# Performance work log

Measured on AMD Instinct MI355X. Metric: run time of the kernel, lower is better.

## Reference

```python
import jax, jax.numpy as jnp
import numpy as np

B, T, C, H = 8, 2048, 1024, 64

def setup_inputs() -> dict:
    key = jax.random.key(0)
    k1, k2, k3, k4 = jax.random.split(key, 4)
    x = jax.random.normal(k1, (B, T, C), dtype=jnp.float32)
    # torch nn.Linear default init ~ U(-1/sqrt(in), 1/sqrt(in)); scale kept small for stability
    s = 1.0 / np.sqrt(C)
    Wq = jax.random.uniform(k2, (C, H), dtype=jnp.float32, minval=-s, maxval=s)
    Wk = jax.random.uniform(k3, (C, H), dtype=jnp.float32, minval=-s, maxval=s)
    Wv = jax.random.uniform(k4, (C, H), dtype=jnp.float32, minval=-s, maxval=s)
    return {"x": x, "Wq": Wq, "Wk": Wk, "Wv": Wv}

def reference(x, Wq, Wk, Wv):
    # x: [B,T,C]; Wq/Wk/Wv: [C,H] (equivalent to torch Linear weight transposed)
    Q = jnp.einsum('btc,ch->bth', x, Wq)
    K = jnp.einsum('btc,ch->bth', x, Wk)
    V = jnp.einsum('btc,ch->bth', x, Wv)
    H_ = Q.shape[-1]
    scale = 1.0 / jnp.sqrt(jnp.asarray(H_, dtype=Q.dtype))
    w = jnp.einsum('bqh,bkh->bqk', Q, K) * scale  # [B,T,T]
    T_ = x.shape[1]
    causal = jnp.tril(jnp.ones((T_, T_), dtype=bool))
    w = jnp.where(causal, w, -jnp.inf)
    w = jax.nn.softmax(w, axis=-1)
    out = jnp.einsum('bqk,bkh->bqh', w, V)  # [B,T,H]
    return out
```

## Files before the change

kernel.cpp:

```cpp
#include <hip/hip_runtime.h>
#include <math.h>

#define Bb 8
#define Tt 2048
#define Cc 1024
#define Hh 64
#define BT (Bb * Tt)
#define SLOG2E 0.18033688011112042f

typedef __attribute__((ext_vector_type(8))) short short8;
typedef __attribute__((ext_vector_type(4))) float floatx4;

__device__ inline unsigned short f2bf(float f) {
  unsigned int u = __builtin_bit_cast(unsigned int, f);
  u += 0x7fff + ((u >> 16) & 1);
  return (unsigned short)(u >> 16);
}
__device__ inline float bf2f(unsigned short u) {
  unsigned int x = ((unsigned int)u) << 16;
  return __builtin_bit_cast(float, x);
}

__global__ __launch_bounds__(256) void wconv2(
    const float* __restrict__ Wq, const float* __restrict__ Wk,
    const float* __restrict__ Wv, unsigned short* __restrict__ WTf) {
  int bid = blockIdx.x;
  int w = bid >> 5;
  int kc = bid & 31;
  const float* __restrict__ W = (w == 0) ? Wq : (w == 1 ? Wk : Wv);
  int t = threadIdx.x;
  int hg = t >> 6, quad = (t >> 4) & 3, lrow = t & 15;
  int g = w * 4 + hg;
  int h = hg * 16 + lrow;
  unsigned short tmp[8];
#pragma unroll
  for (int j = 0; j < 8; ++j)
    tmp[j] = f2bf(W[(size_t)(kc * 32 + quad * 8 + j) * Hh + h]);
  unsigned short* dst = &WTf[((size_t)(g * 32 + kc) * 64 + quad * 16 + lrow) * 8];
  *(ushort4*)dst = make_ushort4(tmp[0], tmp[1], tmp[2], tmp[3]);
  *(ushort4*)(dst + 4) = make_ushort4(tmp[4], tmp[5], tmp[6], tmp[7]);
}

__global__ __launch_bounds__(256) void qkv5(
    const float* __restrict__ x, const unsigned short* __restrict__ WTf,
    unsigned short* __restrict__ Qb, unsigned short* __restrict__ Kb,
    unsigned short* __restrict__ VTt) {
  __shared__ __align__(16) unsigned short Af[2048];

  int mt = blockIdx.x;
  int t = threadIdx.x;
  int wv = t >> 6, lane = t & 63;
  int lrow = lane & 15, quad = lane >> 4;

  floatx4 acc[2][3];
#pragma unroll
  for (int g2 = 0; g2 < 2; ++g2)
#pragma unroll
    for (int j = 0; j < 3; ++j)
#pragma unroll
      for (int r = 0; r < 4; ++r) acc[g2][j][r] = 0.f;

  int srow = t >> 3, scg = t & 7;
  int skc2 = scg >> 2, squad = scg & 3;
  int sslot = ((srow >> 4) * 2 + skc2) * 64 + squad * 16 +
              (((srow & 15) + squad + 4 * skc2) & 15);
  const float* xp = x + (size_t)(mt * 32 + srow) * Cc + scg * 8;

  int aslot[2][2];
#pragma unroll
  for (int g2 = 0; g2 < 2; ++g2)
#pragma unroll
    for (int kc2 = 0; kc2 < 2; ++kc2)
      aslot[g2][kc2] = ((g2 * 2 + kc2) * 64 + quad * 16 +
                        ((lrow + quad + 4 * kc2) & 15)) * 8;

  const unsigned short* wbase[3];
#pragma unroll
  for (int j = 0; j < 3; ++j)
    wbase[j] = WTf + (size_t)(wv * 3 + j) * 32 * 512 + lane * 8;

  float4 nv0 = *(const float4*)xp;
  float4 nv1 = *(const float4*)(xp + 4);

  for (int kk = 0; kk < 16; ++kk) {
    __syncthreads();
    short8 a;
    a[0] = (short)f2bf(nv0.x); a[1] = (short)f2bf(nv0.y);
    a[2] = (short)f2bf(nv0.z); a[3] = (short)f2bf(nv0.w);
    a[4] = (short)f2bf(nv1.x); a[5] = (short)f2bf(nv1.y);
    a[6] = (short)f2bf(nv1.z); a[7] = (short)f2bf(nv1.w);
    *(short8*)&Af[sslot * 8] = a;
    if (kk < 15) {
      nv0 = *(const float4*)(xp + (kk + 1) * 64);
      nv1 = *(const float4*)(xp + (kk + 1) * 64 + 4);
    }
    __syncthreads();

    short8 bf[3][2];
    int kg = kk * 2;
#pragma unroll
    for (int j = 0; j < 3; ++j)
#pragma unroll
      for (int kc2 = 0; kc2 < 2; ++kc2)
        bf[j][kc2] = *(const short8*)(wbase[j] + (size_t)(kg + kc2) * 512);
    short8 af[2][2];
#pragma unroll
    for (int g2 = 0; g2 < 2; ++g2)
#pragma unroll
      for (int kc2 = 0; kc2 < 2; ++kc2)
        af[g2][kc2] = *(const short8*)&Af[aslot[g2][kc2]];
#pragma unroll
    for (int g2 = 0; g2 < 2; ++g2)
#pragma unroll
      for (int j = 0; j < 3; ++j) {
        acc[g2][j] = __builtin_amdgcn_mfma_f32_16x16x32_bf16(af[g2][0], bf[j][0], acc[g2][j], 0, 0, 0);
        acc[g2][j] = __builtin_amdgcn_mfma_f32_16x16x32_bf16(af[g2][1], bf[j][1], acc[g2][j], 0, 0, 0);
      }
  }

#pragma unroll
  for (int g2 = 0; g2 < 2; ++g2) {
    int tok0 = mt * 32 + g2 * 16 + quad * 4;
#pragma unroll
    for (int j = 0; j < 3; ++j) {
      int nbase = (wv * 3 + j) * 16;
      if (nbase >= 128) {
        int h = nbase - 128 + lrow;
        *(ushort4*)&VTt[(size_t)(tok0 >> 6) * 4096 + h * 64 + (tok0 & 63)] =
            make_ushort4(f2bf(acc[g2][j][0]), f2bf(acc[g2][j][1]),
                         f2bf(acc[g2][j][2]), f2bf(acc[g2][j][3]));
      } else {
        unsigned short* dst = (nbase >= 64) ? Kb : Qb;
        int col = (nbase & 63) + lrow;
#pragma unroll
        for (int r = 0; r < 4; ++r)
          dst[(size_t)(tok0 + r) * Hh + col] = f2bf(acc[g2][j][r]);
      }
    }
  }
}

__global__ __launch_bounds__(512) void attn3(
    const unsigned short* __restrict__ Qb, const unsigned short* __restrict__ Kb,
    const unsigned short* __restrict__ VTt, float* __restrict__ out) {
  __shared__ __align__(16) unsigned char smem[33 * 1024];
  unsigned short* Pall = (unsigned short*)smem;
  unsigned short* Ocomb = (unsigned short*)smem;
  float* Lcomb = (float*)(smem + 32768);

  int bid = blockIdx.x;
  int b = bid >> 5;
  int j = bid & 31;
  int t = threadIdx.x;
  int wv = t >> 6, lane = t & 63;
  int lrow = lane & 15, quad = lane >> 4;

  unsigned short* Pw = Pall + wv * 2048;

  short8 ones;
#pragma unroll
  for (int i = 0; i < 8; ++i) ones[i] = (short)0x3F80;

  for (int half = 0; half < 2; ++half) {
    int qt = half ? (63 - j) : j;
    int q0 = qt * 32;
    int nkt = (qt >> 1) + 1;

    short8 aq[2][2];
#pragma unroll
    for (int qs = 0; qs < 2; ++qs)
#pragma unroll
      for (int kc = 0; kc < 2; ++kc)
        aq[qs][kc] = *(const short8*)
            &Qb[(size_t)(b * Tt + q0 + qs * 16 + lrow) * Hh + kc * 32 + quad * 8];

    floatx4 acc_o[2][4];
    floatx4 acc_l[2];
#pragma unroll
    for (int qs = 0; qs < 2; ++qs) {
#pragma unroll
      for (int r = 0; r < 4; ++r) acc_l[qs][r] = 0.f;
#pragma unroll
      for (int hs = 0; hs < 4; ++hs)
#pragma unroll
        for (int r = 0; r < 4; ++r) acc_o[qs][hs][r] = 0.f;
    }

    for (int kt = wv; kt < nkt; kt += 8) {
      int kbase = b * Tt + kt * 64;
      short8 kf[4][2], vf[4][2];
#pragma unroll
      for (int sn = 0; sn < 4; ++sn)
#pragma unroll
        for (int kc = 0; kc < 2; ++kc)
          kf[sn][kc] = *(const short8*)
              &Kb[(size_t)(kbase + sn * 16 + lrow) * Hh + kc * 32 + quad * 8];
      int ktile = b * 32 + kt;
#pragma unroll
      for (int hs = 0; hs < 4; ++hs)
#pragma unroll
        for (int kc = 0; kc < 2; ++kc)
          vf[hs][kc] = *(const short8*)
              &VTt[(size_t)ktile * 4096 + (hs * 16 + lrow) * 64 + kc * 32 + quad * 8];

      floatx4 s[2][4];
#pragma unroll
      for (int qs = 0; qs < 2; ++qs)
#pragma unroll
        for (int sn = 0; sn < 4; ++sn) {
          floatx4 z;
#pragma unroll
          for (int r = 0; r < 4; ++r) z[r] = 0.f;
          z = __builtin_amdgcn_mfma_f32_16x16x32_bf16(aq[qs][0], kf[sn][0], z, 0, 0, 0);
          z = __builtin_amdgcn_mfma_f32_16x16x32_bf16(aq[qs][1], kf[sn][1], z, 0, 0, 0);
          s[qs][sn] = z;
        }

      bool diag = (kt == nkt - 1);
#pragma unroll
      for (int qs = 0; qs < 2; ++qs)
#pragma unroll
        for (int sn = 0; sn < 4; ++sn) {
          int k5 = (sn & 1) * 16 + lrow;
          int slot = qs * 2 + (sn >> 1);
          int rlbase = (k5 >> 3) * 16;
#pragma unroll
          for (int r = 0; r < 4; ++r) {
            float v = s[qs][sn][r] * SLOG2E;
            if (diag) {
              int gk = kt * 64 + sn * 16 + lrow;
              int gq = q0 + qs * 16 + quad * 4 + r;
              if (gk > gq) v = -INFINITY;
            }
            float p = exp2f(v);
            Pw[slot * 512 + (rlbase + quad * 4 + r) * 8 + (k5 & 7)] = f2bf(p);
          }
        }

      short8 ap[2][2];
#pragma unroll
      for (int qs = 0; qs < 2; ++qs)
#pragma unroll
        for (int kc = 0; kc < 2; ++kc)
          ap[qs][kc] = *(const short8*)&Pw[(qs * 2 + kc) * 512 + lane * 8];

#pragma unroll
      for (int qs = 0; qs < 2; ++qs) {
        acc_l[qs] = __builtin_amdgcn_mfma_f32_16x16x32_bf16(ap[qs][0], ones, acc_l[qs], 0, 0, 0);
        acc_l[qs] = __builtin_amdgcn_mfma_f32_16x16x32_bf16(ap[qs][1], ones, acc_l[qs], 0, 0, 0);
#pragma unroll
        for (int hs = 0; hs < 4; ++hs) {
          acc_o[qs][hs] = __builtin_amdgcn_mfma_f32_16x16x32_bf16(ap[qs][0], vf[hs][0], acc_o[qs][hs], 0, 0, 0);
          acc_o[qs][hs] = __builtin_amdgcn_mfma_f32_16x16x32_bf16(ap[qs][1], vf[hs][1], acc_o[qs][hs], 0, 0, 0);
        }
      }
    }

#pragma unroll
    for (int qs = 0; qs < 2; ++qs)
#pragma unroll
      for (int hs = 0; hs < 4; ++hs) {
        int s8 = qs * 4 + hs;
        *(ushort4*)&Ocomb[((wv * 8 + s8) * 64 + lane) * 4] =
            make_ushort4(f2bf(acc_o[qs][hs][0]), f2bf(acc_o[qs][hs][1]),
                         f2bf(acc_o[qs][hs][2]), f2bf(acc_o[qs][hs][3]));
      }
    if (lrow == 0) {
#pragma unroll
      for (int qs = 0; qs < 2; ++qs)
#pragma unroll
        for (int r = 0; r < 4; ++r)
          Lcomb[wv * 32 + qs * 16 + quad * 4 + r] = acc_l[qs][r];
    }
    __syncthreads();

    {
      int qsub = wv >> 2, hs = wv & 3;
      float o[4] = {0.f, 0.f, 0.f, 0.f};
#pragma unroll
      for (int w = 0; w < 8; ++w) {
        ushort4 pk = *(const ushort4*)&Ocomb[((w * 8 + wv) * 64 + lane) * 4];
        o[0] += bf2f(pk.x); o[1] += bf2f(pk.y);
        o[2] += bf2f(pk.z); o[3] += bf2f(pk.w);
      }
#pragma unroll
      for (int r = 0; r < 4; ++r) {
        float lv = 0.f;
#pragma unroll
        for (int w = 0; w < 8; ++w)
          lv += Lcomb[w * 32 + qsub * 16 + quad * 4 + r];
        int row = q0 + qsub * 16 + quad * 4 + r;
        out[(size_t)(b * Tt + row) * Hh + hs * 16 + lrow] = o[r] / lv;
      }
    }
    __syncthreads();
  }
}

extern "C" void kernel_launch(void* const* d_in, const int* in_sizes, int n_in,
                              void* d_out, int out_size, void* d_ws, size_t ws_size,
                              hipStream_t stream) {
  const float* x = (const float*)d_in[0];
  const float* Wq = (const float*)d_in[1];
  const float* Wk = (const float*)d_in[2];
  const float* Wv = (const float*)d_in[3];
  float* out = (float*)d_out;

  unsigned short* WTf = (unsigned short*)d_ws;
  unsigned short* Qb = WTf + 192 * 1024;
  unsigned short* Kb = Qb + (size_t)BT * Hh;
  unsigned short* VTt = Kb + (size_t)BT * Hh;

  wconv2<<<dim3(96), dim3(256), 0, stream>>>(Wq, Wk, Wv, WTf);
  qkv5<<<dim3(512), dim3(256), 0, stream>>>(x, WTf, Qb, Kb, VTt);
  attn3<<<dim3(256), dim3(512), 0, stream>>>(Qb, Kb, VTt, out);
}
```

Before: 132.8 us.

## Prefetch two x tiles, use packed bf16 converts, transpose-read P, fold softmax scale

```diff
diff --git a/kernel.cpp b/kernel.cpp
--- a/kernel.cpp
+++ b/kernel.cpp
@@ -9,7 +9,9 @@
 #define SLOG2E 0.18033688011112042f
 
 typedef __attribute__((ext_vector_type(8))) short short8;
+typedef __attribute__((ext_vector_type(4))) short s16x4;
 typedef __attribute__((ext_vector_type(4))) float floatx4;
+typedef __attribute__((ext_vector_type(4))) unsigned int uint4v;
 
 __device__ inline unsigned short f2bf(float f) {
   unsigned int u = __builtin_bit_cast(unsigned int, f);
@@ -79,20 +81,28 @@
   for (int j = 0; j < 3; ++j)
     wbase[j] = WTf + (size_t)(wv * 3 + j) * 32 * 512 + lane * 8;
 
-  float4 nv0 = *(const float4*)xp;
-  float4 nv1 = *(const float4*)(xp + 4);
-
-  for (int kk = 0; kk < 16; ++kk) {
+  float4 va0 = *(const float4*)xp;
+  float4 va1 = *(const float4*)(xp + 4);
+  float4 vb0 = *(const float4*)(xp + 64);
+  float4 vb1 = *(const float4*)(xp + 68);
+
+  auto cvt8 = [](const float4& u, const float4& v) -> short8 {
+    unsigned int p0, p1, p2, p3;
+    asm("v_cvt_pk_bf16_f32 %0, %1, %2" : "=v"(p0) : "v"(u.x), "v"(u.y));
+    asm("v_cvt_pk_bf16_f32 %0, %1, %2" : "=v"(p1) : "v"(u.z), "v"(u.w));
+    asm("v_cvt_pk_bf16_f32 %0, %1, %2" : "=v"(p2) : "v"(v.x), "v"(v.y));
+    asm("v_cvt_pk_bf16_f32 %0, %1, %2" : "=v"(p3) : "v"(v.z), "v"(v.w));
+    uint4v w; w[0] = p0; w[1] = p1; w[2] = p2; w[3] = p3;
+    return __builtin_bit_cast(short8, w);
+  };
+
+  auto step = [&](float4& n0, float4& n1, int kk) {
     __syncthreads();
-    short8 a;
-    a[0] = (short)f2bf(nv0.x); a[1] = (short)f2bf(nv0.y);
-    a[2] = (short)f2bf(nv0.z); a[3] = (short)f2bf(nv0.w);
-    a[4] = (short)f2bf(nv1.x); a[5] = (short)f2bf(nv1.y);
-    a[6] = (short)f2bf(nv1.z); a[7] = (short)f2bf(nv1.w);
+    short8 a = cvt8(n0, n1);
     *(short8*)&Af[sslot * 8] = a;
-    if (kk < 15) {
-      nv0 = *(const float4*)(xp + (kk + 1) * 64);
-      nv1 = *(const float4*)(xp + (kk + 1) * 64 + 4);
+    if (kk + 2 < 16) {
+      n0 = *(const float4*)(xp + (kk + 2) * 64);
+      n1 = *(const float4*)(xp + (kk + 2) * 64 + 4);
     }
     __syncthreads();
 
@@ -116,6 +126,12 @@
         acc[g2][j] = __builtin_amdgcn_mfma_f32_16x16x32_bf16(af[g2][0], bf[j][0], acc[g2][j], 0, 0, 0);
         acc[g2][j] = __builtin_amdgcn_mfma_f32_16x16x32_bf16(af[g2][1], bf[j][1], acc[g2][j], 0, 0, 0);
       }
+  };
+
+#pragma unroll
+  for (int kk2 = 0; kk2 < 8; ++kk2) {
+    step(va0, va1, kk2 * 2);
+    step(vb0, vb1, kk2 * 2 + 1);
   }
 
 #pragma unroll
@@ -131,10 +147,11 @@
                          f2bf(acc[g2][j][2]), f2bf(acc[g2][j][3]));
       } else {
         unsigned short* dst = (nbase >= 64) ? Kb : Qb;
+        float sc = (nbase >= 64) ? 1.0f : SLOG2E;
         int col = (nbase & 63) + lrow;
 #pragma unroll
         for (int r = 0; r < 4; ++r)
-          dst[(size_t)(tok0 + r) * Hh + col] = f2bf(acc[g2][j][r]);
+          dst[(size_t)(tok0 + r) * Hh + col] = f2bf(acc[g2][j][r] * sc);
       }
     }
   }
@@ -156,6 +173,16 @@
   int lrow = lane & 15, quad = lane >> 4;
 
   unsigned short* Pw = Pall + wv * 2048;
+  unsigned int pbase = (unsigned int)(size_t)Pw;
+
+  unsigned int paddr[2][2];
+#pragma unroll
+  for (int qs = 0; qs < 2; ++qs)
+#pragma unroll
+    for (int kc = 0; kc < 2; ++kc)
+      paddr[qs][kc] = pbase + (unsigned int)(qs * 2048 + kc * 1024 + quad * 256 + lrow * 8);
+
+  int wbase_off = (lrow >> 2) * 64 + (lrow & 3) * 16 + quad * 4;
 
   short8 ones;
 #pragma unroll
@@ -204,6 +231,7 @@
               &VTt[(size_t)ktile * 4096 + (hs * 16 + lrow) * 64 + kc * 32 + quad * 8];
 
       floatx4 s[2][4];
+      __builtin_amdgcn_s_setprio(1);
 #pragma unroll
       for (int qs = 0; qs < 2; ++qs)
 #pragma unroll
@@ -215,35 +243,48 @@
           z = __builtin_amdgcn_mfma_f32_16x16x32_bf16(aq[qs][1], kf[sn][1], z, 0, 0, 0);
           s[qs][sn] = z;
         }
+      __builtin_amdgcn_s_setprio(0);
 
       bool diag = (kt == nkt - 1);
 #pragma unroll
       for (int qs = 0; qs < 2; ++qs)
 #pragma unroll
         for (int sn = 0; sn < 4; ++sn) {
-          int k5 = (sn & 1) * 16 + lrow;
-          int slot = qs * 2 + (sn >> 1);
-          int rlbase = (k5 >> 3) * 16;
+          float p[4];
 #pragma unroll
           for (int r = 0; r < 4; ++r) {
-            float v = s[qs][sn][r] * SLOG2E;
+            float v = s[qs][sn][r];
             if (diag) {
               int gk = kt * 64 + sn * 16 + lrow;
               int gq = q0 + qs * 16 + quad * 4 + r;
               if (gk > gq) v = -INFINITY;
             }
-            float p = exp2f(v);
-            Pw[slot * 512 + (rlbase + quad * 4 + r) * 8 + (k5 & 7)] = f2bf(p);
+            p[r] = __builtin_amdgcn_exp2f(v);
           }
+          unsigned int w0, w1;
+          asm("v_cvt_pk_bf16_f32 %0, %1, %2" : "=v"(w0) : "v"(p[0]), "v"(p[1]));
+          asm("v_cvt_pk_bf16_f32 %0, %1, %2" : "=v"(w1) : "v"(p[2]), "v"(p[3]));
+          int woff = qs * 1024 + (sn >> 1) * 512 + (sn & 1) * 256 + wbase_off;
+          *(uint2*)&Pw[woff] = make_uint2(w0, w1);
         }
 
+      asm volatile("s_waitcnt lgkmcnt(0)" ::: "memory");
       short8 ap[2][2];
 #pragma unroll
       for (int qs = 0; qs < 2; ++qs)
 #pragma unroll
-        for (int kc = 0; kc < 2; ++kc)
-          ap[qs][kc] = *(const short8*)&Pw[(qs * 2 + kc) * 512 + lane * 8];
-
+        for (int kc = 0; kc < 2; ++kc) {
+          s16x4 lo, hi;
+          asm volatile("ds_read_b64_tr_b16 %0, %1"
+                       : "=v"(lo) : "v"(paddr[qs][kc]) : "memory");
+          asm volatile("ds_read_b64_tr_b16 %0, %1 offset:128"
+                       : "=v"(hi) : "v"(paddr[qs][kc]) : "memory");
+          ap[qs][kc] = __builtin_shufflevector(lo, hi, 0, 1, 2, 3, 4, 5, 6, 7);
+        }
+      asm volatile("s_waitcnt lgkmcnt(0)" ::: "memory");
+      __builtin_amdgcn_sched_barrier(0);
+
+      __builtin_amdgcn_s_setprio(1);
 #pragma unroll
       for (int qs = 0; qs < 2; ++qs) {
         acc_l[qs] = __builtin_amdgcn_mfma_f32_16x16x32_bf16(ap[qs][0], ones, acc_l[qs], 0, 0, 0);
@@ -254,6 +295,7 @@
           acc_o[qs][hs] = __builtin_amdgcn_mfma_f32_16x16x32_bf16(ap[qs][1], vf[hs][1], acc_o[qs][hs], 0, 0, 0);
         }
       }
+      __builtin_amdgcn_s_setprio(0);
     }
 
 #pragma unroll
```

Measured after the change: 130.2 us. No clear change (-1.9%).
